# Performance work log

Measured on AMD Instinct MI355X. Metric: run time of the kernel, lower is better.

Reference implementation:

```python
import jax, jax.numpy as jnp
import numpy as np

D_MODEL = 1024
NUM_HEADS = 16
D_K = D_MODEL // NUM_HEADS
B, S = 2, 2048


def setup_inputs() -> dict:
    key = jax.random.key(0)
    ks = jax.random.split(key, 9)
    sc = 1.0 / np.sqrt(D_MODEL)
    return {
        "x": jax.random.normal(ks[0], (B, S, D_MODEL), dtype=jnp.float32),
        "Wq": jax.random.normal(ks[1], (D_MODEL, D_MODEL), dtype=jnp.float32) * sc,
        "bq": jnp.zeros((D_MODEL,), dtype=jnp.float32),
        "Wk": jax.random.normal(ks[2], (D_MODEL, D_MODEL), dtype=jnp.float32) * sc,
        "bk": jnp.zeros((D_MODEL,), dtype=jnp.float32),
        "Wv": jax.random.normal(ks[3], (D_MODEL, D_MODEL), dtype=jnp.float32) * sc,
        "bv": jnp.zeros((D_MODEL,), dtype=jnp.float32),
        "Wo": jax.random.normal(ks[4], (D_MODEL, D_MODEL), dtype=jnp.float32) * sc,
        "bo": jnpp if False else jnp.zeros((D_MODEL,), dtype=jnp.float32),
    }


def reference(x, Wq, bq, Wk, bk, Wv, bv, Wo, bo):
    b, s, d = x.shape
    # projections, split heads: (B, H, S, Dk)
    def heads(t):
        return t.reshape(b, s, NUM_HEADS, D_K).transpose(0, 2, 1, 3)
    Q = heads(x @ Wq + bq)
    K = heads(x @ Wk + bk)
    V = heads(x @ Wv + bv)
    scores = jnp.einsum("bhqd,bhkd->bhqk", Q, K) / jnp.sqrt(jnp.float32(D_K))
    attn = jax.nn.softmax(scores, axis=-1)
    out = jnp.einsum("bhqk,bhkd->bhqd", attn, V)
    out = out.transpose(0, 2, 1, 3).reshape(b, s, d)
    return out @ Wo + bo
```

## Files before the change

kernel.cpp:

```cpp
#include <hip/hip_runtime.h>
#include <hip/hip_bf16.h>


#define SEQ 2048
#define DMODEL 1024
#define NHEAD 16
#define DK 64
#define NBATCH 2
#define NBH 32
#define MTOT 4096

typedef __attribute__((ext_vector_type(4)))  float  f32x4;
typedef __attribute__((ext_vector_type(16))) float  f32x16;
typedef __attribute__((ext_vector_type(8)))  short  bf16x8;
typedef __attribute__((ext_vector_type(4)))  short  bf16x4;
typedef __attribute__((ext_vector_type(4)))  unsigned short u16x4;
typedef __attribute__((ext_vector_type(2)))  unsigned int u32x2;

#define QSCALE 0.18033688f

__device__ __forceinline__ unsigned short f2bf(float x) {
  union { __hip_bfloat16 h; unsigned short u; } cv;
  cv.h = __float2bfloat16(x);
  return cv.u;
}

__device__ __forceinline__ unsigned cvtpk(float lo, float hi) {
  unsigned r;
  asm("v_cvt_pk_bf16_f32 %0, %1, %2" : "=v"(r) : "v"(lo), "v"(hi));
  return r;
}

#define EXP2(x) __builtin_amdgcn_exp2f(x)

__device__ __forceinline__ float fmax3(float a, float b, float c) {
  return fmaxf(fmaxf(a, b), c);
}

__device__ __forceinline__ void gload16(const void* g, void* l) {
  __builtin_amdgcn_global_load_lds(
      (const __attribute__((address_space(1))) unsigned int*)g,
      (__attribute__((address_space(3))) unsigned int*)l, 16, 0, 0);
}

__global__ __launch_bounds__(256) void conv_all(
    const float* __restrict__ X, unsigned short* __restrict__ Xb,
    const float* __restrict__ W0, const float* __restrict__ W1,
    const float* __restrict__ W2, const float* __restrict__ W3,
    unsigned short* __restrict__ T0, unsigned short* __restrict__ T1,
    unsigned short* __restrict__ T2, unsigned short* __restrict__ T3) {
  __shared__ float tile[64][65];
  const int b = blockIdx.x;
  if (b >= 1024) {
    size_t i = ((size_t)(b - 1024) * 256 + threadIdx.x) * 16;
#pragma unroll
    for (int c = 0; c < 4; ++c) {
      f32x4 v = *(const f32x4*)&X[i + c * 4];
      u16x4 pk;
      pk[0] = f2bf(v[0]); pk[1] = f2bf(v[1]);
      pk[2] = f2bf(v[2]); pk[3] = f2bf(v[3]);
      *(u16x4*)&Xb[i + c * 4] = pk;
    }
    return;
  }
  const int z = b >> 8, rem = b & 255;
  const float* W; unsigned short* T;
  switch (z) {
    case 0: W = W0; T = T0; break;
    case 1: W = W1; T = T1; break;
    case 2: W = W2; T = T2; break;
    default: W = W3; T = T3; break;
  }
  const int k0 = (rem & 15) * 64, n0 = (rem >> 4) * 64;
  const int tr = threadIdx.x >> 4, tc = (threadIdx.x & 15) * 4;
#pragma unroll
  for (int i = 0; i < 4; ++i) {
    int r = tr + i * 16;
    f32x4 v = *(const f32x4*)&W[(size_t)(k0 + r) * DMODEL + n0 + tc];
    tile[r][tc + 0] = v[0]; tile[r][tc + 1] = v[1];
    tile[r][tc + 2] = v[2]; tile[r][tc + 3] = v[3];
  }
  __syncthreads();
#pragma unroll
  for (int i = 0; i < 4; ++i) {
    int nr = tr + i * 16;
    u16x4 pk;
    pk[0] = f2bf(tile[tc + 0][nr]); pk[1] = f2bf(tile[tc + 1][nr]);
    pk[2] = f2bf(tile[tc + 2][nr]); pk[3] = f2bf(tile[tc + 3][nr]);
    *(u16x4*)&T[(size_t)(n0 + nr) * DMODEL + k0 + tc] = pk;
  }
}

__global__ __launch_bounds__(256) void gemm_qkv(
    const short* __restrict__ A, const short* __restrict__ Bt,
    const float* __restrict__ bq, const float* __restrict__ bk,
    const float* __restrict__ bv, unsigned short* __restrict__ Qg,
    unsigned short* __restrict__ Kg, unsigned short* __restrict__ Vtg) {
  const int tid = threadIdx.x;
  const int lane = tid & 63, w = tid >> 6;
  const int lq = lane & 15, g = lane >> 4;
  const int bidg = blockIdx.x;
  const int j = bidg >> 3;
  const int n_t = (bidg & 7) * 3 + (j % 3);
  const int m0 = (j / 3) * 128, n0 = n_t * 128;
  const int wm = (w >> 1) * 64, wn = (w & 1) * 64;
  const int which = n0 >> 10;

  __shared__ __attribute__((aligned(16))) short abuf[128 * 64];
  __shared__ __attribute__((aligned(16))) short bbuf[128 * 64];

  f32x4 acc[4][4] = {};
  const char* Ab = (const char*)A;
  const char* Bb = (const char*)Bt;

  if (which == 2) {
    for (int kt = 0; kt < 16; ++kt) {
      __syncthreads();
#pragma unroll
      for (int i = 0; i < 4; ++i) {
        int y = tid * 16 + i * 4096;
        int row = y >> 7, cb = y & 127;
        gload16(Ab + (size_t)(m0 + row) * 2048 + kt * 128 + cb, (char*)abuf + y);
        gload16(Bb + (size_t)(n0 + row) * 2048 + kt * 128 + cb, (char*)bbuf + y);
      }
      __syncthreads();
#pragma unroll
      for (int ks = 0; ks < 2; ++ks) {
        bf16x8 af[4], bfr[4];
#pragma unroll
        for (int i = 0; i < 4; ++i) {
          af[i]  = *(const bf16x8*)&abuf[(wm + i * 16 + lq) * 64 + ks * 32 + g * 8];
          bfr[i] = *(const bf16x8*)&bbuf[(wn + i * 16 + lq) * 64 + ks * 32 + g * 8];
        }
#pragma unroll
        for (int mi = 0; mi < 4; ++mi)
#pragma unroll
          for (int ni = 0; ni < 4; ++ni)
            acc[mi][ni] = __builtin_amdgcn_mfma_f32_16x16x32_bf16(
                af[mi], bfr[ni], acc[mi][ni], 0, 0, 0);
      }
    }
#pragma unroll
    for (int mi = 0; mi < 4; ++mi) {
#pragma unroll
      for (int ni = 0; ni < 4; ++ni) {
        const int nl = (n0 & 1023) + wn + ni * 16 + lq;
        const int mbase = m0 + wm + mi * 16 + g * 4;
        const float bs = bv[nl];
        const int h = nl >> 6, d = nl & 63;
        const int b = mbase >> 11, s = mbase & 2047;
        u16x4 pk;
#pragma unroll
        for (int r = 0; r < 4; ++r) pk[r] = f2bf(acc[mi][ni][r] + bs);
        *(u16x4*)&Vtg[(size_t)((b * NHEAD + h) * DK + d) * SEQ + s] = pk;
      }
    }
  } else {
    for (int kt = 0; kt < 16; ++kt) {
      __syncthreads();
#pragma unroll
      for (int i = 0; i < 4; ++i) {
        int y = tid * 16 + i * 4096;
        int row = y >> 7, cb = y & 127;
        gload16(Ab + (size_t)(m0 + row) * 2048 + kt * 128 + cb, (char*)abuf + y);
        gload16(Bb + (size_t)(n0 + row) * 2048 + kt * 128 + cb, (char*)bbuf + y);
      }
      __syncthreads();
#pragma unroll
      for (int ks = 0; ks < 2; ++ks) {
        bf16x8 af[4], bfr[4];
#pragma unroll
        for (int i = 0; i < 4; ++i) {
          af[i]  = *(const bf16x8*)&abuf[(wm + i * 16 + lq) * 64 + ks * 32 + g * 8];
          bfr[i] = *(const bf16x8*)&bbuf[(wn + i * 16 + lq) * 64 + ks * 32 + g * 8];
        }
#pragma unroll
        for (int mi = 0; mi < 4; ++mi)
#pragma unroll
          for (int ni = 0; ni < 4; ++ni)
            acc[mi][ni] = __builtin_amdgcn_mfma_f32_16x16x32_bf16(
                bfr[ni], af[mi], acc[mi][ni], 0, 0, 0);
      }
    }
    const float* bias = (which == 0) ? bq : bk;
    unsigned short* o = (which == 0) ? Qg : Kg;
    const float sc = (which == 0) ? QSCALE : 1.0f;
#pragma unroll
    for (int mi = 0; mi < 4; ++mi) {
#pragma unroll
      for (int ni = 0; ni < 4; ++ni) {
        const int nlb = (n0 & 1023) + wn + ni * 16 + g * 4;
        const int m = m0 + wm + mi * 16 + lq;
        const int b = m >> 11, s = m & 2047;
        const int h = nlb >> 6, d = nlb & 63;
        const f32x4 bsv = *(const f32x4*)&bias[nlb];
        u16x4 pk;
#pragma unroll
        for (int r = 0; r < 4; ++r)
          pk[r] = f2bf((acc[mi][ni][r] + bsv[r]) * sc);
        *(u16x4*)&o[(size_t)((b * NHEAD + h) * SEQ + s) * DK + d] = pk;
      }
    }
  }
}

__global__ __launch_bounds__(256) void gemm_out(const short* __restrict__ A,
                                                const short* __restrict__ Bt,
                                                const float* __restrict__ bias,
                                                float* __restrict__ o) {
  const int tid = threadIdx.x;
  const int lane = tid & 63, w = tid >> 6;
  const int lq = lane & 15, g = lane >> 4;
  const int m0 = (blockIdx.x >> 3) * 128, n0 = (blockIdx.x & 7) * 128;
  const int wm = (w >> 1) * 64, wn = (w & 1) * 64;

  __shared__ __attribute__((aligned(16))) short abuf[128 * 64];
  __shared__ __attribute__((aligned(16))) short bbuf[128 * 64];

  f32x4 acc[4][4] = {};
  const char* Ab = (const char*)A;
  const char* Bb = (const char*)Bt;

  for (int kt = 0; kt < 16; ++kt) {
    __syncthreads();
#pragma unroll
    for (int i = 0; i < 4; ++i) {
      int y = tid * 16 + i * 4096;
      int row = y >> 7, cb = y & 127;
      gload16(Ab + (size_t)(m0 + row) * 2048 + kt * 128 + cb, (char*)abuf + y);
      gload16(Bb + (size_t)(n0 + row) * 2048 + kt * 128 + cb, (char*)bbuf + y);
    }
    __syncthreads();
#pragma unroll
    for (int ks = 0; ks < 2; ++ks) {
      bf16x8 af[4], bfr[4];
#pragma unroll
      for (int i = 0; i < 4; ++i) {
        af[i]  = *(const bf16x8*)&abuf[(wm + i * 16 + lq) * 64 + ks * 32 + g * 8];
        bfr[i] = *(const bf16x8*)&bbuf[(wn + i * 16 + lq) * 64 + ks * 32 + g * 8];
      }
#pragma unroll
      for (int mi = 0; mi < 4; ++mi)
#pragma unroll
        for (int ni = 0; ni < 4; ++ni)
          acc[mi][ni] = __builtin_amdgcn_mfma_f32_16x16x32_bf16(
              af[mi], bfr[ni], acc[mi][ni], 0, 0, 0);
    }
  }

#pragma unroll
  for (int mi = 0; mi < 4; ++mi) {
#pragma unroll
    for (int ni = 0; ni < 4; ++ni) {
      const int n = n0 + wn + ni * 16 + lq;
      const int mbase = m0 + wm + mi * 16 + g * 4;
      const float bs = bias[n];
#pragma unroll
      for (int r = 0; r < 4; ++r)
        o[(size_t)(mbase + r) * DMODEL + n] = acc[mi][ni][r] + bs;
    }
  }
}

__global__ __launch_bounds__(128) void attn_kernel(
    const short* __restrict__ Qg, const short* __restrict__ Kg,
    const short* __restrict__ Vtg, unsigned short* __restrict__ Og) {
  const int tid = threadIdx.x, w = tid >> 6;
  const int lane = tid & 63;
  const int l5 = lane & 31, hi = lane >> 5;
  const int sw7 = l5 & 7, hi8 = hi * 8;
  const int bid = blockIdx.x;
  const int swz = (bid & 7) * 128 + (bid >> 3);
  const int bh = swz >> 5, q0 = (swz & 31) * 64;

  __shared__ __attribute__((aligned(16))) short kbuf[2][64 * 64];
  __shared__ __attribute__((aligned(16))) short vbuf[2][64 * 64];

  const short* qrow = Qg + ((size_t)bh * SEQ + q0 + w * 32 + l5) * DK;
  bf16x8 qf[4];
#pragma unroll
  for (int ds = 0; ds < 4; ++ds)
    qf[ds] = *(const bf16x8*)&qrow[ds * 16 + hi8];

  bf16x8 ones;
#pragma unroll
  for (int jj = 0; jj < 8; ++jj) ones[jj] = (short)0x3F80;

  f32x16 oacc0 = {}, oacc1 = {};
  float m_run = -3.0e38f, l_run = 0.f;

  const char* kbase = (const char*)(Kg + (size_t)bh * SEQ * DK);
  const char* vbase = (const char*)(Vtg + (size_t)bh * DK * SEQ);

  int ksrcA[4], vsrcA[4], ydstA[4];
#pragma unroll
  for (int i = 0; i < 4; ++i) {
    const int y = tid * 16 + i * 2048;
    const int r = y >> 7;
    const int c = (y ^ (r << 4)) & 0x70;
    ydstA[i] = y;
    ksrcA[i] = (y & ~0x70) | c;
    vsrcA[i] = r * 4096 + c;
  }

#define STAGE(T, BI)                                                       \
  do {                                                                     \
    _Pragma("unroll")                                                      \
    for (int i = 0; i < 4; ++i) {                                          \
      gload16(kbase + (size_t)(T) * 8192 + ksrcA[i],                       \
              (char*)kbuf[BI] + ydstA[i]);                                 \
      gload16(vbase + vsrcA[i] + (size_t)(T) * 128,                        \
              (char*)vbuf[BI] + ydstA[i]);                                 \
    }                                                                      \
  } while (0)

  STAGE(0, 0);

  for (int t = 0; t < 32; ++t) {
    const int bi = t & 1;
    __syncthreads();
    if (t < 31) STAGE(t + 1, bi ^ 1);

    const char* kb = (const char*)kbuf[bi];
    const char* vb = (const char*)vbuf[bi];

    f32x16 s0 = {}, s1 = {};
    __builtin_amdgcn_s_setprio(1);
#pragma unroll
    for (int ds = 0; ds < 4; ++ds) {
      const int ch = ((ds * 2 + hi) ^ sw7) << 4;
      bf16x8 kf0 = *(const bf16x8*)(kb + l5 * 128 + ch);
      bf16x8 kf1 = *(const bf16x8*)(kb + (32 + l5) * 128 + ch);
      s0 = __builtin_amdgcn_mfma_f32_32x32x16_bf16(kf0, qf[ds], s0, 0, 0, 0);
      s1 = __builtin_amdgcn_mfma_f32_32x32x16_bf16(kf1, qf[ds], s1, 0, 0, 0);
    }
    __builtin_amdgcn_s_setprio(0);

    float t0 = fmax3(s0[0], s0[1], s0[2]);
    float t1 = fmax3(s0[3], s0[4], s0[5]);
    float t2 = fmax3(s0[6], s0[7], s0[8]);
    float t3 = fmax3(s0[9], s0[10], s0[11]);
    float t4 = fmax3(s0[12], s0[13], s0[14]);
    float t5 = fmax3(s1[0], s1[1], s1[2]);
    float t6 = fmax3(s1[3], s1[4], s1[5]);
    float t7 = fmax3(s1[6], s1[7], s1[8]);
    float t8 = fmax3(s1[9], s1[10], s1[11]);
    float t9 = fmax3(s1[12], s1[13], s1[14]);
    float u0 = fmax3(t0, t1, t2);
    float u1 = fmax3(t3, t4, s0[15]);
    float u2 = fmax3(t5, t6, t7);
    float u3 = fmax3(t8, t9, s1[15]);
    float lm = fmaxf(fmax3(u0, u1, u2), u3);

    if (!__all(lm <= m_run + 8.0f)) {
      float vm = fmaxf(lm, __shfl_xor(lm, 32));
      const float mn = fmaxf(m_run, vm);
      const float cr = EXP2(m_run - mn);
#pragma unroll
      for (int r = 0; r < 16; ++r) { oacc0[r] *= cr; oacc1[r] *= cr; }
      l_run *= cr;
      m_run = mn;
    }

#pragma unroll
    for (int r = 0; r < 16; ++r) {
      s0[r] = EXP2(s0[r] - m_run);
      s1[r] = EXP2(s1[r] - m_run);
    }

    f32x16 ls = {};
    __builtin_amdgcn_s_setprio(1);
#pragma unroll
    for (int ks = 0; ks < 4; ++ks) {
      const f32x16& ss = (ks < 2) ? s0 : s1;
      const int b = (ks & 1) * 8;
      unsigned A0 = cvtpk(ss[b + 0], ss[b + 1]);
      unsigned A1 = cvtpk(ss[b + 4], ss[b + 5]);
      unsigned B0 = cvtpk(ss[b + 2], ss[b + 3]);
      unsigned B1 = cvtpk(ss[b + 6], ss[b + 7]);
      u32x2 ra = __builtin_amdgcn_permlane32_swap(A0, A1, false, false);
      u32x2 rb = __builtin_amdgcn_permlane32_swap(B0, B1, false, false);
      union { unsigned u[4]; bf16x8 v; } pf;
      pf.u[0] = ra[0]; pf.u[1] = rb[0]; pf.u[2] = ra[1]; pf.u[3] = rb[1];

      const int ch = ((ks * 2 + hi) ^ sw7) << 4;
      ls = __builtin_amdgcn_mfma_f32_32x32x16_bf16(ones, pf.v, ls, 0, 0, 0);
      bf16x8 vf0 = *(const bf16x8*)(vb + l5 * 128 + ch);
      bf16x8 vf1 = *(const bf16x8*)(vb + (32 + l5) * 128 + ch);
      oacc0 = __builtin_amdgcn_mfma_f32_32x32x16_bf16(vf0, pf.v, oacc0, 0, 0, 0);
      oacc1 = __builtin_amdgcn_mfma_f32_32x32x16_bf16(vf1, pf.v, oacc1, 0, 0, 0);
    }
    __builtin_amdgcn_s_setprio(0);
    l_run += ls[0];
  }
#undef STAGE

  const float inv = 1.0f / l_run;
  const int bb = bh >> 4, h = bh & 15;
  const size_t base =
      ((size_t)bb * SEQ + q0 + w * 32 + l5) * DMODEL + h * DK + hi * 4;
#pragma unroll
  for (int c = 0; c < 4; ++c) {
    u16x4 pk0, pk1;
#pragma unroll
    for (int b = 0; b < 4; ++b) {
      pk0[b] = f2bf(oacc0[4 * c + b] * inv);
      pk1[b] = f2bf(oacc1[4 * c + b] * inv);
    }
    *(u16x4*)&Og[base + 8 * c] = pk0;
    *(u16x4*)&Og[base + 32 + 8 * c] = pk1;
  }
}

extern "C" void kernel_launch(void* const* d_in, const int* in_sizes, int n_in,
                              void* d_out, int out_size, void* d_ws,
                              size_t ws_size, hipStream_t stream) {
  const float* x  = (const float*)d_in[0];
  const float* Wq = (const float*)d_in[1];
  const float* bq = (const float*)d_in[2];
  const float* Wk = (const float*)d_in[3];
  const float* bk = (const float*)d_in[4];
  const float* Wv = (const float*)d_in[5];
  const float* bv = (const float*)d_in[6];
  const float* Wo = (const float*)d_in[7];
  const float* bo = (const float*)d_in[8];
  float* out = (float*)d_out;

  char* ws = (char*)d_ws;
  unsigned short* Xb    = (unsigned short*)(ws);
  unsigned short* Wtqkv = (unsigned short*)(ws + (8u << 20));
  unsigned short* Wto   = (unsigned short*)(ws + (14u << 20));
  unsigned short* Qg    = (unsigned short*)(ws + (16u << 20));
  unsigned short* Kg    = (unsigned short*)(ws + (24u << 20));
  unsigned short* Vtg   = (unsigned short*)(ws + (32u << 20));
  unsigned short* Ab    = Xb;

  conv_all<<<dim3(2048), 256, 0, stream>>>(
      x, Xb, Wq, Wk, Wv, Wo,
      Wtqkv, Wtqkv + (1u << 20), Wtqkv + (2u << 20), Wto);

  gemm_qkv<<<dim3(768), 256, 0, stream>>>(
      (const short*)Xb, (const short*)Wtqkv, bq, bk, bv, Qg, Kg, Vtg);

  attn_kernel<<<dim3(1024), 128, 0, stream>>>(
      (const short*)Qg, (const short*)Kg, (const short*)Vtg, Ab);

  gemm_out<<<dim3(256), 256, 0, stream>>>(
      (const short*)Ab, (const short*)Wto, bo, out);
}
```

Measured before the change: 143.5 us.

## Enlarge attention tiles to 128 queries and 128 keys per block

Each attention block now has four waves covering 128 query rows and processes 128-key K/V tiles per iteration, halving both the grid size and the number of loop iterations. Staged K/V tiles are shared by twice as many waves, which cuts global-to-LDS traffic per query and halves the barriers and rescale checks per key. In exchange, LDS use per block doubles and each wave holds four score accumulators, so register pressure rises and occupancy may drop. Only 512 blocks are launched, which may underfill the GPU.

```diff
diff --git a/kernel.cpp b/kernel.cpp
--- a/kernel.cpp
+++ b/kernel.cpp
@@ -35,6 +35,15 @@
 
 __device__ __forceinline__ float fmax3(float a, float b, float c) {
   return fmaxf(fmaxf(a, b), c);
+}
+
+__device__ __forceinline__ float vmax16(const f32x16& v) {
+  float a = fmax3(v[0], v[1], v[2]);
+  float b = fmax3(v[3], v[4], v[5]);
+  float c = fmax3(v[6], v[7], v[8]);
+  float d = fmax3(v[9], v[10], v[11]);
+  float e = fmax3(v[12], v[13], v[14]);
+  return fmaxf(fmax3(a, b, c), fmax3(d, e, v[15]));
 }
 
 __device__ __forceinline__ void gload16(const void* g, void* l) {
@@ -262,19 +271,19 @@
   }
 }
 
-__global__ __launch_bounds__(128) void attn_kernel(
+__global__ __launch_bounds__(256) void attn_kernel(
     const short* __restrict__ Qg, const short* __restrict__ Kg,
     const short* __restrict__ Vtg, unsigned short* __restrict__ Og) {
-  const int tid = threadIdx.x, w = tid >> 6;
-  const int lane = tid & 63;
+  const int tid = threadIdx.x, lane = tid & 63, w = tid >> 6;
   const int l5 = lane & 31, hi = lane >> 5;
   const int sw7 = l5 & 7, hi8 = hi * 8;
+  const int sw = sw7 << 4;
   const int bid = blockIdx.x;
-  const int swz = (bid & 7) * 128 + (bid >> 3);
-  const int bh = swz >> 5, q0 = (swz & 31) * 64;
-
-  __shared__ __attribute__((aligned(16))) short kbuf[2][64 * 64];
-  __shared__ __attribute__((aligned(16))) short vbuf[2][64 * 64];
+  const int swz = (bid & 7) * 64 + (bid >> 3);
+  const int bh = swz >> 4, q0 = (swz & 15) * 128;
+
+  __shared__ __attribute__((aligned(16))) short kbuf[2][128 * 64];
+  __shared__ __attribute__((aligned(16))) short vbuf[2][64 * 128];
 
   const short* qrow = Qg + ((size_t)bh * SEQ + q0 + w * 32 + l5) * DK;
   bf16x8 qf[4];
@@ -292,65 +301,58 @@
   const char* kbase = (const char*)(Kg + (size_t)bh * SEQ * DK);
   const char* vbase = (const char*)(Vtg + (size_t)bh * DK * SEQ);
 
-  int ksrcA[4], vsrcA[4], ydstA[4];
+  int kdst[4], ksrc[4], vsrc[4];
 #pragma unroll
   for (int i = 0; i < 4; ++i) {
-    const int y = tid * 16 + i * 2048;
-    const int r = y >> 7;
-    const int c = (y ^ (r << 4)) & 0x70;
-    ydstA[i] = y;
-    ksrcA[i] = (y & ~0x70) | c;
-    vsrcA[i] = r * 4096 + c;
+    const int y = tid * 16 + i * 4096;
+    kdst[i] = y;
+    { const int r = y >> 7;
+      const int c = (y ^ (r << 4)) & 0x70;
+      ksrc[i] = (y & ~0x70) | c; }
+    { const int r = y >> 8;
+      const int scol = ((y ^ (r << 4)) & 0x70) | (y & 0x80);
+      vsrc[i] = r * 4096 + scol; }
   }
 
 #define STAGE(T, BI)                                                       \
   do {                                                                     \
     _Pragma("unroll")                                                      \
     for (int i = 0; i < 4; ++i) {                                          \
-      gload16(kbase + (size_t)(T) * 8192 + ksrcA[i],                       \
-              (char*)kbuf[BI] + ydstA[i]);                                 \
-      gload16(vbase + vsrcA[i] + (size_t)(T) * 128,                        \
-              (char*)vbuf[BI] + ydstA[i]);                                 \
+      gload16(kbase + (size_t)(T) * 16384 + ksrc[i],                       \
+              (char*)kbuf[BI] + kdst[i]);                                  \
+      gload16(vbase + (size_t)(T) * 256 + vsrc[i],                         \
+              (char*)vbuf[BI] + kdst[i]);                                  \
     }                                                                      \
   } while (0)
 
   STAGE(0, 0);
 
-  for (int t = 0; t < 32; ++t) {
+  for (int t = 0; t < 16; ++t) {
     const int bi = t & 1;
     __syncthreads();
-    if (t < 31) STAGE(t + 1, bi ^ 1);
+    if (t < 15) STAGE(t + 1, bi ^ 1);
 
     const char* kb = (const char*)kbuf[bi];
     const char* vb = (const char*)vbuf[bi];
 
-    f32x16 s0 = {}, s1 = {};
+    f32x16 s0 = {}, s1 = {}, s2 = {}, s3 = {};
     __builtin_amdgcn_s_setprio(1);
 #pragma unroll
     for (int ds = 0; ds < 4; ++ds) {
       const int ch = ((ds * 2 + hi) ^ sw7) << 4;
-      bf16x8 kf0 = *(const bf16x8*)(kb + l5 * 128 + ch);
+      bf16x8 kf0 = *(const bf16x8*)(kb + (l5) * 128 + ch);
       bf16x8 kf1 = *(const bf16x8*)(kb + (32 + l5) * 128 + ch);
+      bf16x8 kf2 = *(const bf16x8*)(kb + (64 + l5) * 128 + ch);
+      bf16x8 kf3 = *(const bf16x8*)(kb + (96 + l5) * 128 + ch);
       s0 = __builtin_amdgcn_mfma_f32_32x32x16_bf16(kf0, qf[ds], s0, 0, 0, 0);
       s1 = __builtin_amdgcn_mfma_f32_32x32x16_bf16(kf1, qf[ds], s1, 0, 0, 0);
+      s2 = __builtin_amdgcn_mfma_f32_32x32x16_bf16(kf2, qf[ds], s2, 0, 0, 0);
+      s3 = __builtin_amdgcn_mfma_f32_32x32x16_bf16(kf3, qf[ds], s3, 0, 0, 0);
     }
     __builtin_amdgcn_s_setprio(0);
 
-    float t0 = fmax3(s0[0], s0[1], s0[2]);
-    float t1 = fmax3(s0[3], s0[4], s0[5]);
-    float t2 = fmax3(s0[6], s0[7], s0[8]);
-    float t3 = fmax3(s0[9], s0[10], s0[11]);
-    float t4 = fmax3(s0[12], s0[13], s0[14]);
-    float t5 = fmax3(s1[0], s1[1], s1[2]);
-    float t6 = fmax3(s1[3], s1[4], s1[5]);
-    float t7 = fmax3(s1[6], s1[7], s1[8]);
-    float t8 = fmax3(s1[9], s1[10], s1[11]);
-    float t9 = fmax3(s1[12], s1[13], s1[14]);
-    float u0 = fmax3(t0, t1, t2);
-    float u1 = fmax3(t3, t4, s0[15]);
-    float u2 = fmax3(t5, t6, t7);
-    float u3 = fmax3(t8, t9, s1[15]);
-    float lm = fmaxf(fmax3(u0, u1, u2), u3);
+    float lm = fmaxf(fmaxf(vmax16(s0), vmax16(s1)),
+                     fmaxf(vmax16(s2), vmax16(s3)));
 
     if (!__all(lm <= m_run + 8.0f)) {
       float vm = fmaxf(lm, __shfl_xor(lm, 32));
@@ -366,13 +368,15 @@
     for (int r = 0; r < 16; ++r) {
       s0[r] = EXP2(s0[r] - m_run);
       s1[r] = EXP2(s1[r] - m_run);
+      s2[r] = EXP2(s2[r] - m_run);
+      s3[r] = EXP2(s3[r] - m_run);
     }
 
     f32x16 ls = {};
     __builtin_amdgcn_s_setprio(1);
 #pragma unroll
-    for (int ks = 0; ks < 4; ++ks) {
-      const f32x16& ss = (ks < 2) ? s0 : s1;
+    for (int ks = 0; ks < 8; ++ks) {
+      const f32x16& ss = (ks < 2) ? s0 : (ks < 4) ? s1 : (ks < 6) ? s2 : s3;
       const int b = (ks & 1) * 8;
       unsigned A0 = cvtpk(ss[b + 0], ss[b + 1]);
       unsigned A1 = cvtpk(ss[b + 4], ss[b + 5]);
@@ -383,10 +387,10 @@
       union { unsigned u[4]; bf16x8 v; } pf;
       pf.u[0] = ra[0]; pf.u[1] = rb[0]; pf.u[2] = ra[1]; pf.u[3] = rb[1];
 
-      const int ch = ((ks * 2 + hi) ^ sw7) << 4;
+      const int ch = ((ks * 2 + hi) << 4) ^ sw;
       ls = __builtin_amdgcn_mfma_f32_32x32x16_bf16(ones, pf.v, ls, 0, 0, 0);
-      bf16x8 vf0 = *(const bf16x8*)(vb + l5 * 128 + ch);
-      bf16x8 vf1 = *(const bf16x8*)(vb + (32 + l5) * 128 + ch);
+      bf16x8 vf0 = *(const bf16x8*)(vb + (l5) * 256 + ch);
+      bf16x8 vf1 = *(const bf16x8*)(vb + (32 + l5) * 256 + ch);
       oacc0 = __builtin_amdgcn_mfma_f32_32x32x16_bf16(vf0, pf.v, oacc0, 0, 0, 0);
       oacc1 = __builtin_amdgcn_mfma_f32_32x32x16_bf16(vf1, pf.v, oacc1, 0, 0, 0);
     }
@@ -442,7 +446,7 @@
   gemm_qkv<<<dim3(768), 256, 0, stream>>>(
       (const short*)Xb, (const short*)Wtqkv, bq, bk, bv, Qg, Kg, Vtg);
 
-  attn_kernel<<<dim3(1024), 128, 0, stream>>>(
+  attn_kernel<<<dim3(512), 256, 0, stream>>>(
       (const short*)Qg, (const short*)Kg, (const short*)Vtg, Ab);
 
   gemm_out<<<dim3(256), 256, 0, stream>>>(
```

Result: slower. 158.1 us (+10.1%).
